# Kernel tuning notes

Measured on AMD Instinct MI355X. Metric: run time of the kernel, lower is better.

The kernel has to match this reference:

```python
import jax, jax.numpy as jnp
import numpy as np

DIM = 1024
NUM_HEADS = 16
SCALE = DIM ** (-0.5)  # NOTE: source scales by full dim, not head_dim


def setup_inputs() -> dict:
    key = jax.random.key(0)
    ks = jax.random.split(key, 10)
    B, N, C = 2, 2048, DIM
    s = 0.02
    return {
        "x": jax.random.normal(ks[0], (B, N, C), dtype=jnp.float32),
        "queries": jax.random.normal(ks[1], (B, N, C), dtype=jnp.float32),
        "wq": jax.random.normal(ks[2], (C, C), dtype=jnp.float32) * s,
        "bq": jnp.zeros((C,), dtype=jnp.float32),
        "wk": jax.random.normal(ks[3], (C, C), dtype=jnp.float32) * s,
        "bk": jnp.zeros((C,), dtype=jnp.float32),
        "wv": jax.random.normal(ks[4], (C, C), dtype=jnp.float32) * s,
        "bv": jnp.zeros((C,), dtype=jnp.float32),
        "wo": jax.random.normal(ks[5], (C, C), dtype=jnp.float32) * s,
        "bo": jnp.zeros((C,), dtype=jnp.float32),
    }


def reference(x, queries, wq, bq, wk, bk, wv, bv, wo, bo):
    B, N, C = queries.shape
    H = NUM_HEADS
    D = C // H
    # torch Linear: y = x @ W.T + b  (W is [out, in])
    q = (queries @ wq.T + bq).reshape(B, N, H, D).transpose(0, 2, 1, 3)  # [B,H,N,D]
    k = (x @ wk.T + bk).reshape(B, N, H, D).transpose(0, 2, 1, 3)
    v = (x @ wv.T + bv).reshape(B, N, H, D).transpose(0, 2, 1, 3)
    attn = jnp.einsum("bhqd,bhkd->bhqk", q, k) * SCALE  # full-dim scale per source
    attn = jax.nn.softmax(attn, axis=-1)
    out = jnp.einsum("bhqk,bhkd->bhqd", attn, v)  # [B,H,N,D]
    out = out.transpose(0, 2, 1, 3).reshape(B, N, C)
    return out @ wo.T + bo
```

## Files before the change

### kernel.cpp

```cpp
#include <hip/hip_runtime.h>
#include <hip/hip_bf16.h>

typedef __attribute__((ext_vector_type(8))) short bf16x8;
typedef __attribute__((ext_vector_type(4))) float f32x4;
typedef unsigned short u16;
typedef unsigned int u32;

#define MFMA16(a,b,c) __builtin_amdgcn_mfma_f32_16x16x32_bf16((a),(b),(c),0,0,0)

#if defined(__has_builtin) && __has_builtin(__builtin_amdgcn_exp2f)
#define EXP2(x) __builtin_amdgcn_exp2f(x)
#else
#define EXP2(x) exp2f(x)
#endif

#define QSCALE 0.045084220027780106f

__device__ __forceinline__ u16 f2bf(float f) {
  union { float f; unsigned int u; } v; v.f = f;
  unsigned int r = v.u + 0x7FFFu + ((v.u >> 16) & 1u);
  return (u16)(r >> 16);
}

__device__ __forceinline__ u32 pkbf(float a, float b) {
  union { __hip_bfloat162 h; u32 u; } cv;
  cv.h = __float22bfloat162_rn(make_float2(a, b));
  return cv.u;
}

__device__ __forceinline__ void gld16(const void* g, void* l) {
  __builtin_amdgcn_global_load_lds(
      (__attribute__((address_space(1))) void*)(g),
      (__attribute__((address_space(3))) void*)(l), 16, 0, 0);
}

__global__ __launch_bounds__(256) void cast_all(
    const float* __restrict__ x, const float* __restrict__ qu,
    const float* __restrict__ wq, const float* __restrict__ wk,
    const float* __restrict__ wv, const float* __restrict__ wo,
    u16* __restrict__ xb, u16* __restrict__ qub,
    u16* __restrict__ wqb, u16* __restrict__ wkb,
    u16* __restrict__ wvb, u16* __restrict__ wob)
{
  int i = blockIdx.x * 256 + threadIdx.x;
  const float4* src; u16* dst; int off;
  if (i < 1048576)      { src = (const float4*)qu; dst = qub; off = i; }
  else if (i < 2097152) { src = (const float4*)x;  dst = xb;  off = i - 1048576; }
  else if (i < 2359296) { src = (const float4*)wq; dst = wqb; off = i - 2097152; }
  else if (i < 2621440) { src = (const float4*)wk; dst = wkb; off = i - 2359296; }
  else if (i < 2883584) { src = (const float4*)wv; dst = wvb; off = i - 2621440; }
  else                  { src = (const float4*)wo; dst = wob; off = i - 2883584; }
  float4 v = src[off];
  ushort4 r; r.x = f2bf(v.x); r.y = f2bf(v.y); r.z = f2bf(v.z); r.w = f2bf(v.w);
  ((ushort4*)dst)[off] = r;
}

__global__ __launch_bounds__(256) void gemm_qkv(
    const u16* __restrict__ qub, const u16* __restrict__ xb,
    const u16* __restrict__ wqb, const u16* __restrict__ wkb, const u16* __restrict__ wvb,
    const float* __restrict__ bq, const float* __restrict__ bk, const float* __restrict__ bv,
    u16* __restrict__ qhd, u16* __restrict__ khd, u16* __restrict__ vtd)
{
  __shared__ u16 sm2[2 * 128 * 64];
  u16* As = sm2;
  u16* Bs = sm2 + 128 * 64;
  int tid = threadIdx.x, w = tid >> 6, lane = tid & 63;
  int c = lane & 15, quad = lane >> 4;
  int bm = blockIdx.x, bn = blockIdx.y, z = blockIdx.z;
  int wm = w >> 1, wn = w & 1;
  const u16* A = (z == 0) ? qub : xb;
  const u16* W = (z == 0) ? wqb : (z == 1) ? wkb : wvb;
  f32x4 acc[4][4] = {};
  for (int k0 = 0; k0 < 1024; k0 += 64) {
#pragma unroll
    for (int i = 0; i < 4; i++) {
      int seg = i * 256 + w * 64 + lane;
      int row = seg >> 3, pseg = seg & 7;
      int lseg = pseg ^ (row & 7);
      gld16(A + (size_t)(bm * 128 + row) * 1024 + k0 + lseg * 8,
            &As[(i * 256 + w * 64) * 8]);
      gld16(W + (size_t)(bn * 128 + row) * 1024 + k0 + lseg * 8,
            &Bs[(i * 256 + w * 64) * 8]);
    }
    __syncthreads();
#pragma unroll
    for (int ks = 0; ks < 2; ks++) {
      bf16x8 af[4], bfr[4];
#pragma unroll
      for (int mt = 0; mt < 4; mt++) {
        int row = wm * 64 + mt * 16 + c;
        int cseg = (ks * 4 + quad) ^ (row & 7);
        af[mt] = *(const bf16x8*)&As[(row * 8 + cseg) * 8];
      }
#pragma unroll
      for (int nt = 0; nt < 4; nt++) {
        int row = wn * 64 + nt * 16 + c;
        int cseg = (ks * 4 + quad) ^ (row & 7);
        bfr[nt] = *(const bf16x8*)&Bs[(row * 8 + cseg) * 8];
      }
#pragma unroll
      for (int mt = 0; mt < 4; mt++)
#pragma unroll
        for (int nt = 0; nt < 4; nt++)
          acc[mt][nt] = MFMA16(af[mt], bfr[nt], acc[mt][nt]);
    }
    __syncthreads();
  }
  if (z < 2) {
    const float* bias = (z == 0) ? bq : bk;
    u16* dst = (z == 0) ? qhd : khd;
#pragma unroll
    for (int nt = 0; nt < 4; nt++) {
      int o = bn * 128 + wn * 64 + nt * 16 + c;
      float bval = bias[o];
      int h = o >> 6, d = o & 63;
#pragma unroll
      for (int mt = 0; mt < 4; mt++)
#pragma unroll
        for (int j = 0; j < 4; j++) {
          int m = bm * 128 + wm * 64 + mt * 16 + quad * 4 + j;
          int b = m >> 11, n = m & 2047;
          float val = acc[mt][nt][j] + bval;
          if (z == 0)
            dst[((size_t)(b * 16 + h) * 2048 + n) * 64 + d] = f2bf(val * QSCALE);
          else
            dst[((size_t)(b * 16 + h) * 2048 + n) * 64 + d] = f2bf(val);
        }
    }
  } else {
    u16* LT = sm2;
    for (int h2 = 0; h2 < 2; h2++) {
      if (wm == h2) {
#pragma unroll
        for (int nt = 0; nt < 4; nt++) {
          int o = bn * 128 + wn * 64 + nt * 16 + c;
          float bval = bv[o];
          int col = wn * 64 + nt * 16 + c;
#pragma unroll
          for (int mt = 0; mt < 4; mt++)
#pragma unroll
            for (int j = 0; j < 4; j++) {
              int rl = mt * 16 + quad * 4 + j;
              int krl = (rl & 32) | ((rl & 12) << 1) | ((rl & 16) >> 2) | (rl & 3);
              LT[krl * 137 + col] = f2bf(acc[mt][nt][j] + bval);
            }
        }
      }
      __syncthreads();
      int m0 = bm * 128 + h2 * 64;
      int b = m0 >> 11, n0 = m0 & 2047;
      int tk0 = (tid & 7) * 8;
#pragma unroll
      for (int pass = 0; pass < 4; pass++) {
        int cl = pass * 32 + (tid >> 3);
        int o = bn * 128 + cl, hh = o >> 6, dd = o & 63;
        u16 tmp[8];
#pragma unroll
        for (int i = 0; i < 8; i++) tmp[i] = LT[(tk0 + i) * 137 + cl];
        uint4 pk4;
        pk4.x = ((u32)tmp[1] << 16) | tmp[0];
        pk4.y = ((u32)tmp[3] << 16) | tmp[2];
        pk4.z = ((u32)tmp[5] << 16) | tmp[4];
        pk4.w = ((u32)tmp[7] << 16) | tmp[6];
        *(uint4*)(vtd + ((size_t)(b * 16 + hh) * 64 + dd) * 2048 + n0 + tk0) = pk4;
      }
      __syncthreads();
    }
  }
}

__global__ __launch_bounds__(256) void attn(
    const u16* __restrict__ qh, const u16* __restrict__ kh,
    const u16* __restrict__ vt, u16* __restrict__ ot)
{
  __shared__ u16 Kbuf[2][64 * 64];
  __shared__ u16 Vbuf[2][64 * 64];
  int tid = threadIdx.x, w = tid >> 6, lane = tid & 63;
  int c = lane & 15, quad = lane >> 4;
  int qt = blockIdx.x, bh = blockIdx.y;
  const u16* qp = qh + ((size_t)bh * 2048 + qt * 128 + w * 32) * 64;

  bf16x8 Qf[2][2];
#pragma unroll
  for (int qt2 = 0; qt2 < 2; qt2++)
#pragma unroll
    for (int ks = 0; ks < 2; ks++)
      Qf[qt2][ks] = *(const bf16x8*)(qp + (size_t)(qt2 * 16 + c) * 64 + ks * 32 + quad * 8);

  int off0 = c * 64 + ((quad) ^ (c & 7)) * 8;
  int off1 = c * 64 + ((4 + quad) ^ (c & 7)) * 8;

  int srow = tid >> 3;
  int sls  = (tid & 7) ^ (srow & 7);
  const u16* kg0 = kh + (size_t)bh * 2048 * 64 + srow * 64 + sls * 8;
  const u16* kg1 = kg0 + 32 * 64;
  const u16* vg0 = vt + (size_t)bh * 64 * 2048 + srow * 2048 + sls * 8;
  const u16* vg1 = vg0 + 32 * 2048;
  u16* kd0[2] = {&Kbuf[0][(w * 64) * 8],       &Kbuf[1][(w * 64) * 8]};
  u16* kd1[2] = {&Kbuf[0][(256 + w * 64) * 8], &Kbuf[1][(256 + w * 64) * 8]};
  u16* vd0[2] = {&Vbuf[0][(w * 64) * 8],       &Vbuf[1][(w * 64) * 8]};
  u16* vd1[2] = {&Vbuf[0][(256 + w * 64) * 8], &Vbuf[1][(256 + w * 64) * 8]};

  gld16(kg0, kd0[0]); gld16(kg1, kd1[0]);
  gld16(vg0, vd0[0]); gld16(vg1, vd1[0]);
  kg0 += 4096; kg1 += 4096; vg0 += 64; vg1 += 64;
  __syncthreads();

  f32x4 O[2][4] = {};
  f32x4 Lacc[2] = {};
  bf16x8 vone;
#pragma unroll
  for (int j = 0; j < 8; j++) vone[j] = (short)0x3F80;

#define ITER(PH, PREF)                                                          \
  {                                                                             \
    if (PREF) {                                                                 \
      gld16(kg0, kd0[PH ^ 1]); gld16(kg1, kd1[PH ^ 1]);                         \
      gld16(vg0, vd0[PH ^ 1]); gld16(vg1, vd1[PH ^ 1]);                         \
      kg0 += 4096; kg1 += 4096; vg0 += 64; vg1 += 64;                           \
    }                                                                           \
    const u16* Ks = Kbuf[PH];                                                   \
    const u16* Vs = Vbuf[PH];                                                   \
    bf16x8 Kf[4][2];                                                            \
    _Pragma("unroll") for (int nt = 0; nt < 4; nt++) {                          \
      Kf[nt][0] = *(const bf16x8*)&Ks[off0 + nt * 1024];                        \
      Kf[nt][1] = *(const bf16x8*)&Ks[off1 + nt * 1024];                        \
    }                                                                           \
    f32x4 S[2][4] = {};                                                         \
    _Pragma("unroll") for (int qt2 = 0; qt2 < 2; qt2++)                         \
      _Pragma("unroll") for (int nt = 0; nt < 4; nt++) {                        \
        S[qt2][nt] = MFMA16(Kf[nt][0], Qf[qt2][0], S[qt2][nt]);                 \
        S[qt2][nt] = MFMA16(Kf[nt][1], Qf[qt2][1], S[qt2][nt]);                 \
      }                                                                         \
    bf16x8 pa[2][2];                                                            \
    _Pragma("unroll") for (int qt2 = 0; qt2 < 2; qt2++)                         \
      _Pragma("unroll") for (int i = 0; i < 2; i++) {                           \
        float e0 = EXP2(S[qt2][2 * i][0]), e1 = EXP2(S[qt2][2 * i][1]);         \
        float e2 = EXP2(S[qt2][2 * i][2]), e3 = EXP2(S[qt2][2 * i][3]);         \
        float e4 = EXP2(S[qt2][2 * i + 1][0]), e5 = EXP2(S[qt2][2 * i + 1][1]); \
        float e6 = EXP2(S[qt2][2 * i + 1][2]), e7 = EXP2(S[qt2][2 * i + 1][3]); \
        union { uint4 u; bf16x8 v; } cv;                                        \
        cv.u.x = pkbf(e0, e1); cv.u.y = pkbf(e2, e3);                           \
        cv.u.z = pkbf(e4, e5); cv.u.w = pkbf(e6, e7);                           \
        pa[qt2][i] = cv.v;                                                      \
      }                                                                         \
    Lacc[0] = MFMA16(pa[0][0], vone, Lacc[0]);                                  \
    Lacc[0] = MFMA16(pa[0][1], vone, Lacc[0]);                                  \
    Lacc[1] = MFMA16(pa[1][0], vone, Lacc[1]);                                  \
    Lacc[1] = MFMA16(pa[1][1], vone, Lacc[1]);                                  \
    bf16x8 Vf[4][2];                                                            \
    _Pragma("unroll") for (int dt = 0; dt < 4; dt++) {                          \
      Vf[dt][0] = *(const bf16x8*)&Vs[off0 + dt * 1024];                        \
      Vf[dt][1] = *(const bf16x8*)&Vs[off1 + dt * 1024];                        \
    }                                                                           \
    _Pragma("unroll") for (int qt2 = 0; qt2 < 2; qt2++)                         \
      _Pragma("unroll") for (int dt = 0; dt < 4; dt++) {                        \
        O[qt2][dt] = MFMA16(pa[qt2][0], Vf[dt][0], O[qt2][dt]);                 \
        O[qt2][dt] = MFMA16(pa[qt2][1], Vf[dt][1], O[qt2][dt]);                 \
      }                                                                         \
    __syncthreads();                                                            \
  }

  for (int kt2 = 0; kt2 < 15; kt2++) {
    ITER(0, 1)
    ITER(1, 1)
  }
  ITER(0, 1)
  ITER(1, 0)
#undef ITER

  int b_ = bh >> 4, h = bh & 15;
#pragma unroll
  for (int qt2 = 0; qt2 < 2; qt2++) {
    f32x4 linv;
#pragma unroll
    for (int j = 0; j < 4; j++) linv[j] = 1.0f / Lacc[qt2][j];
#pragma unroll
    for (int j = 0; j < 4; j++) {
      int n = qt * 128 + w * 32 + qt2 * 16 + quad * 4 + j;
      u16* op = ot + (((size_t)b_ * 2048 + n) * 16 + h) * 64;
#pragma unroll
      for (int dt = 0; dt < 4; dt++)
        op[dt * 16 + c] = f2bf(O[qt2][dt][j] * linv[j]);
    }
  }
}

__global__ __launch_bounds__(256) void gemm_out(
    const u16* __restrict__ Aot, const u16* __restrict__ wob,
    const float* __restrict__ bo, float* __restrict__ out)
{
  __shared__ u16 As[64 * 64];
  __shared__ u16 Bs[128 * 64];
  int tid = threadIdx.x, w = tid >> 6, lane = tid & 63;
  int bm = blockIdx.x, bn = blockIdx.y;
  int wm = w >> 1, wn = w & 1;
  f32x4 acc[2][4] = {};
  for (int k0 = 0; k0 < 1024; k0 += 64) {
#pragma unroll
    for (int i = 0; i < 2; i++) {
      int seg = i * 256 + tid;
      int row = seg >> 3, pseg = seg & 7;
      int lseg = pseg ^ (row & 7);
      gld16(Aot + (size_t)(bm * 64 + row) * 1024 + k0 + lseg * 8,
            &As[(i * 256 + tid - (tid & 7)) * 8 + (tid & 7) * 8]);
    }
#pragma unroll
    for (int i = 0; i < 4; i++) {
      int seg = i * 256 + tid;
      int row = seg >> 3, pseg = seg & 7;
      int lseg = pseg ^ (row & 7);
      gld16(wob + (size_t)(bn * 128 + row) * 1024 + k0 + lseg * 8,
            &Bs[(i * 256 + tid - (tid & 7)) * 8 + (tid & 7) * 8]);
    }
    __syncthreads();
#pragma unroll
    for (int ks = 0; ks < 2; ks++) {
      bf16x8 af[2], bfr[4];
#pragma unroll
      for (int mt = 0; mt < 2; mt++) {
        int row = wm * 32 + mt * 16 + (lane & 15);
        int cseg = (ks * 4 + (lane >> 4)) ^ (row & 7);
        af[mt] = *(const bf16x8*)&As[(row * 8 + cseg) * 8];
      }
#pragma unroll
      for (int nt = 0; nt < 4; nt++) {
        int row = wn * 64 + nt * 16 + (lane & 15);
        int cseg = (ks * 4 + (lane >> 4)) ^ (row & 7);
        bfr[nt] = *(const bf16x8*)&Bs[(row * 8 + cseg) * 8];
      }
#pragma unroll
      for (int mt = 0; mt < 2; mt++)
#pragma unroll
        for (int nt = 0; nt < 4; nt++)
          acc[mt][nt] = MFMA16(af[mt], bfr[nt], acc[mt][nt]);
    }
    __syncthreads();
  }
#pragma unroll
  for (int nt = 0; nt < 4; nt++) {
    int o = bn * 128 + wn * 64 + nt * 16 + (lane & 15);
    float bval = bo[o];
#pragma unroll
    for (int mt = 0; mt < 2; mt++)
#pragma unroll
      for (int j = 0; j < 4; j++) {
        int m = bm * 64 + wm * 32 + mt * 16 + (lane >> 4) * 4 + j;
        out[(size_t)m * 1024 + o] = acc[mt][nt][j] + bval;
      }
  }
}

extern "C" void kernel_launch(void* const* d_in, const int* in_sizes, int n_in,
                              void* d_out, int out_size, void* d_ws, size_t ws_size,
                              hipStream_t stream)
{
  const float* x  = (const float*)d_in[0];
  const float* qu = (const float*)d_in[1];
  const float* wq = (const float*)d_in[2];
  const float* bq = (const float*)d_in[3];
  const float* wk = (const float*)d_in[4];
  const float* bk = (const float*)d_in[5];
  const float* wv = (const float*)d_in[6];
  const float* bv = (const float*)d_in[7];
  const float* wo = (const float*)d_in[8];
  const float* bo = (const float*)d_in[9];
  float* out = (float*)d_out;
  char* ws = (char*)d_ws;
  u16* xb  = (u16*)(ws + (size_t)0);
  u16* qub = (u16*)(ws + ((size_t)8  << 20));
  u16* wqb = (u16*)(ws + ((size_t)16 << 20));
  u16* wkb = (u16*)(ws + ((size_t)18 << 20));
  u16* wvb = (u16*)(ws + ((size_t)20 << 20));
  u16* wob = (u16*)(ws + ((size_t)22 << 20));
  u16* qhd = (u16*)(ws + ((size_t)24 << 20));
  u16* khd = (u16*)(ws + ((size_t)32 << 20));
  u16* vtd = (u16*)(ws + ((size_t)40 << 20));
  u16* otd = (u16*)(ws + ((size_t)48 << 20));

  cast_all<<<12288, 256, 0, stream>>>(x, qu, wq, wk, wv, wo,
                                      xb, qub, wqb, wkb, wvb, wob);
  gemm_qkv<<<dim3(32, 8, 3), 256, 0, stream>>>(qub, xb, wqb, wkb, wvb,
                                               bq, bk, bv, qhd, khd, vtd);
  attn<<<dim3(16, 32), 256, 0, stream>>>(qhd, khd, vtd, otd);
  gemm_out<<<dim3(64, 8), 256, 0, stream>>>(otd, wob, bo, out);
}
```

Baseline: 209.8 us.

## Vectorize QKV epilogue stores via swapped MFMA operands; shrink attention blocks

For the Q and K projections the MFMA operands are swapped, so each lane holds four consecutive channels and can write packed 8-byte stores instead of scattered 2-byte ones. The scale is folded into an fma with a pre-scaled bias. The V epilogue drops the shared-memory transpose and writes packed token-contiguous chunks straight to the transposed layout, relying on the row permutation in the attention kernel. The attention kernel now uses 128-thread blocks with 64 queries each and a grid ordered with batch-head first, doubling the block count and reusing K/V across neighbouring blocks, at the cost of staging K/V with fewer threads per block.

Result: faster. 204.2 us (-2.7%).

```diff
diff --git a/kernel.cpp b/kernel.cpp
--- a/kernel.cpp
+++ b/kernel.cpp
@@ -61,9 +61,8 @@
     const float* __restrict__ bq, const float* __restrict__ bk, const float* __restrict__ bv,
     u16* __restrict__ qhd, u16* __restrict__ khd, u16* __restrict__ vtd)
 {
-  __shared__ u16 sm2[2 * 128 * 64];
-  u16* As = sm2;
-  u16* Bs = sm2 + 128 * 64;
+  __shared__ u16 As[128 * 64];
+  __shared__ u16 Bs[128 * 64];
   int tid = threadIdx.x, w = tid >> 6, lane = tid & 63;
   int c = lane & 15, quad = lane >> 4;
   int bm = blockIdx.x, bn = blockIdx.y, z = blockIdx.z;
@@ -98,78 +97,75 @@
         int cseg = (ks * 4 + quad) ^ (row & 7);
         bfr[nt] = *(const bf16x8*)&Bs[(row * 8 + cseg) * 8];
       }
-#pragma unroll
-      for (int mt = 0; mt < 4; mt++)
-#pragma unroll
-        for (int nt = 0; nt < 4; nt++)
-          acc[mt][nt] = MFMA16(af[mt], bfr[nt], acc[mt][nt]);
+      if (z < 2) {
+#pragma unroll
+        for (int ct = 0; ct < 4; ct++)
+#pragma unroll
+          for (int tt = 0; tt < 4; tt++)
+            acc[ct][tt] = MFMA16(bfr[ct], af[tt], acc[ct][tt]);
+      } else {
+#pragma unroll
+        for (int mt = 0; mt < 4; mt++)
+#pragma unroll
+          for (int nt = 0; nt < 4; nt++)
+            acc[mt][nt] = MFMA16(af[mt], bfr[nt], acc[mt][nt]);
+      }
     }
     __syncthreads();
   }
   if (z < 2) {
     const float* bias = (z == 0) ? bq : bk;
     u16* dst = (z == 0) ? qhd : khd;
-#pragma unroll
-    for (int nt = 0; nt < 4; nt++) {
-      int o = bn * 128 + wn * 64 + nt * 16 + c;
-      float bval = bias[o];
-      int h = o >> 6, d = o & 63;
-#pragma unroll
-      for (int mt = 0; mt < 4; mt++)
-#pragma unroll
-        for (int j = 0; j < 4; j++) {
-          int m = bm * 128 + wm * 64 + mt * 16 + quad * 4 + j;
-          int b = m >> 11, n = m & 2047;
-          float val = acc[mt][nt][j] + bval;
-          if (z == 0)
-            dst[((size_t)(b * 16 + h) * 2048 + n) * 64 + d] = f2bf(val * QSCALE);
-          else
-            dst[((size_t)(b * 16 + h) * 2048 + n) * 64 + d] = f2bf(val);
-        }
+    float sc = (z == 0) ? QSCALE : 1.0f;
+    float4 bbs[4];
+#pragma unroll
+    for (int ct = 0; ct < 4; ct++) {
+      float4 b4 = *(const float4*)&bias[bn * 128 + wn * 64 + ct * 16 + quad * 4];
+      bbs[ct].x = b4.x * sc; bbs[ct].y = b4.y * sc;
+      bbs[ct].z = b4.z * sc; bbs[ct].w = b4.w * sc;
+    }
+#pragma unroll
+    for (int ct = 0; ct < 4; ct++) {
+      int ch = bn * 128 + wn * 64 + ct * 16 + quad * 4;
+      int h = ch >> 6, d0 = ch & 63;
+#pragma unroll
+      for (int tt = 0; tt < 4; tt++) {
+        int tok = bm * 128 + wm * 64 + tt * 16 + c;
+        int b = tok >> 11, n = tok & 2047;
+        float v0 = fmaf(acc[ct][tt][0], sc, bbs[ct].x);
+        float v1 = fmaf(acc[ct][tt][1], sc, bbs[ct].y);
+        float v2 = fmaf(acc[ct][tt][2], sc, bbs[ct].z);
+        float v3 = fmaf(acc[ct][tt][3], sc, bbs[ct].w);
+        uint2 pk; pk.x = pkbf(v0, v1); pk.y = pkbf(v2, v3);
+        *(uint2*)&dst[((size_t)(b * 16 + h) * 2048 + n) * 64 + d0] = pk;
+      }
     }
   } else {
-    u16* LT = sm2;
-    for (int h2 = 0; h2 < 2; h2++) {
-      if (wm == h2) {
-#pragma unroll
-        for (int nt = 0; nt < 4; nt++) {
-          int o = bn * 128 + wn * 64 + nt * 16 + c;
-          float bval = bv[o];
-          int col = wn * 64 + nt * 16 + c;
-#pragma unroll
-          for (int mt = 0; mt < 4; mt++)
-#pragma unroll
-            for (int j = 0; j < 4; j++) {
-              int rl = mt * 16 + quad * 4 + j;
-              int krl = (rl & 32) | ((rl & 12) << 1) | ((rl & 16) >> 2) | (rl & 3);
-              LT[krl * 137 + col] = f2bf(acc[mt][nt][j] + bval);
-            }
-        }
-      }
-      __syncthreads();
-      int m0 = bm * 128 + h2 * 64;
-      int b = m0 >> 11, n0 = m0 & 2047;
-      int tk0 = (tid & 7) * 8;
-#pragma unroll
-      for (int pass = 0; pass < 4; pass++) {
-        int cl = pass * 32 + (tid >> 3);
-        int o = bn * 128 + cl, hh = o >> 6, dd = o & 63;
-        u16 tmp[8];
-#pragma unroll
-        for (int i = 0; i < 8; i++) tmp[i] = LT[(tk0 + i) * 137 + cl];
-        uint4 pk4;
-        pk4.x = ((u32)tmp[1] << 16) | tmp[0];
-        pk4.y = ((u32)tmp[3] << 16) | tmp[2];
-        pk4.z = ((u32)tmp[5] << 16) | tmp[4];
-        pk4.w = ((u32)tmp[7] << 16) | tmp[6];
-        *(uint4*)(vtd + ((size_t)(b * 16 + hh) * 64 + dd) * 2048 + n0 + tk0) = pk4;
-      }
-      __syncthreads();
-    }
-  }
-}
-
-__global__ __launch_bounds__(256) void attn(
+    float bval[4];
+#pragma unroll
+    for (int nt = 0; nt < 4; nt++)
+      bval[nt] = bv[bn * 128 + wn * 64 + nt * 16 + c];
+#pragma unroll
+    for (int mt = 0; mt < 4; mt++) {
+      int tokl = (mt & 2) * 16 + quad * 8 + (mt & 1) * 4;
+      int tok = bm * 128 + wm * 64 + tokl;
+      int b = tok >> 11, np = tok & 2047;
+#pragma unroll
+      for (int nt = 0; nt < 4; nt++) {
+        int ch = bn * 128 + wn * 64 + nt * 16 + c;
+        int h = ch >> 6, d = ch & 63;
+        float v0 = acc[mt][nt][0] + bval[nt];
+        float v1 = acc[mt][nt][1] + bval[nt];
+        float v2 = acc[mt][nt][2] + bval[nt];
+        float v3 = acc[mt][nt][3] + bval[nt];
+        uint2 pk; pk.x = pkbf(v0, v1); pk.y = pkbf(v2, v3);
+        *(uint2*)&vtd[((size_t)(b * 16 + h) * 64 + d) * 2048 + np] = pk;
+      }
+    }
+  }
+}
+
+__global__ __launch_bounds__(128) void attn(
     const u16* __restrict__ qh, const u16* __restrict__ kh,
     const u16* __restrict__ vt, u16* __restrict__ ot)
 {
@@ -177,8 +173,8 @@
   __shared__ u16 Vbuf[2][64 * 64];
   int tid = threadIdx.x, w = tid >> 6, lane = tid & 63;
   int c = lane & 15, quad = lane >> 4;
-  int qt = blockIdx.x, bh = blockIdx.y;
-  const u16* qp = qh + ((size_t)bh * 2048 + qt * 128 + w * 32) * 64;
+  int bh = blockIdx.x, qt = blockIdx.y;
+  const u16* qp = qh + ((size_t)bh * 2048 + qt * 64 + w * 32) * 64;
 
   bf16x8 Qf[2][2];
 #pragma unroll
@@ -190,20 +186,26 @@
   int off0 = c * 64 + ((quad) ^ (c & 7)) * 8;
   int off1 = c * 64 + ((4 + quad) ^ (c & 7)) * 8;
 
-  int srow = tid >> 3;
-  int sls  = (tid & 7) ^ (srow & 7);
-  const u16* kg0 = kh + (size_t)bh * 2048 * 64 + srow * 64 + sls * 8;
-  const u16* kg1 = kg0 + 32 * 64;
-  const u16* vg0 = vt + (size_t)bh * 64 * 2048 + srow * 2048 + sls * 8;
-  const u16* vg1 = vg0 + 32 * 2048;
-  u16* kd0[2] = {&Kbuf[0][(w * 64) * 8],       &Kbuf[1][(w * 64) * 8]};
-  u16* kd1[2] = {&Kbuf[0][(256 + w * 64) * 8], &Kbuf[1][(256 + w * 64) * 8]};
-  u16* vd0[2] = {&Vbuf[0][(w * 64) * 8],       &Vbuf[1][(w * 64) * 8]};
-  u16* vd1[2] = {&Vbuf[0][(256 + w * 64) * 8], &Vbuf[1][(256 + w * 64) * 8]};
-
-  gld16(kg0, kd0[0]); gld16(kg1, kd1[0]);
-  gld16(vg0, vd0[0]); gld16(vg1, vd1[0]);
-  kg0 += 4096; kg1 += 4096; vg0 += 64; vg1 += 64;
+  int sr = lane >> 3;
+  int row0 = w * 8 + sr;
+  int sls = (lane & 7) ^ (sr & 7);
+  const u16* kg = kh + (size_t)bh * 2048 * 64 + row0 * 64 + sls * 8;
+  const u16* vg = vt + (size_t)bh * 64 * 2048 + row0 * 2048 + sls * 8;
+
+#define STAGE(B)                                                                \
+  {                                                                             \
+    gld16(kg,          &Kbuf[B][(w * 64) * 8]);                                 \
+    gld16(kg + 1024,   &Kbuf[B][(128 + w * 64) * 8]);                           \
+    gld16(kg + 2048,   &Kbuf[B][(256 + w * 64) * 8]);                           \
+    gld16(kg + 3072,   &Kbuf[B][(384 + w * 64) * 8]);                           \
+    gld16(vg,          &Vbuf[B][(w * 64) * 8]);                                 \
+    gld16(vg + 32768,  &Vbuf[B][(128 + w * 64) * 8]);                           \
+    gld16(vg + 65536,  &Vbuf[B][(256 + w * 64) * 8]);                           \
+    gld16(vg + 98304,  &Vbuf[B][(384 + w * 64) * 8]);                           \
+    kg += 4096; vg += 64;                                                       \
+  }
+
+  STAGE(0)
   __syncthreads();
 
   f32x4 O[2][4] = {};
@@ -214,11 +216,7 @@
 
 #define ITER(PH, PREF)                                                          \
   {                                                                             \
-    if (PREF) {                                                                 \
-      gld16(kg0, kd0[PH ^ 1]); gld16(kg1, kd1[PH ^ 1]);                         \
-      gld16(vg0, vd0[PH ^ 1]); gld16(vg1, vd1[PH ^ 1]);                         \
-      kg0 += 4096; kg1 += 4096; vg0 += 64; vg1 += 64;                           \
-    }                                                                           \
+    if (PREF) STAGE(PH ^ 1)                                                     \
     const u16* Ks = Kbuf[PH];                                                   \
     const u16* Vs = Vbuf[PH];                                                   \
     bf16x8 Kf[4][2];                                                            \
@@ -268,6 +266,7 @@
   ITER(0, 1)
   ITER(1, 0)
 #undef ITER
+#undef STAGE
 
   int b_ = bh >> 4, h = bh & 15;
 #pragma unroll
@@ -277,7 +276,7 @@
     for (int j = 0; j < 4; j++) linv[j] = 1.0f / Lacc[qt2][j];
 #pragma unroll
     for (int j = 0; j < 4; j++) {
-      int n = qt * 128 + w * 32 + qt2 * 16 + quad * 4 + j;
+      int n = qt * 64 + w * 32 + qt2 * 16 + quad * 4 + j;
       u16* op = ot + (((size_t)b_ * 2048 + n) * 16 + h) * 64;
 #pragma unroll
       for (int dt = 0; dt < 4; dt++)
@@ -382,6 +381,6 @@
                                       xb, qub, wqb, wkb, wvb, wob);
   gemm_qkv<<<dim3(32, 8, 3), 256, 0, stream>>>(qub, xb, wqb, wkb, wvb,
                                                bq, bk, bv, qhd, khd, vtd);
-  attn<<<dim3(16, 32), 256, 0, stream>>>(qhd, khd, vtd, otd);
+  attn<<<dim3(32, 32), 128, 0, stream>>>(qhd, khd, vtd, otd);
   gemm_out<<<dim3(64, 8), 256, 0, stream>>>(otd, wob, bo, out);
 }
```
